# Kernel optimization log

Measured on AMD Instinct MI355X. Metric: run time of the kernel, lower is better.

Reference implementation:

```python
import math
import jax, jax.numpy as jnp
import numpy as np

# ---- static config ----
B, S, HID = 2, 8192, 1024
H, D = 8, 128                      # num_heads, head_dim = hidden // heads
CHUNK = 128                        # attention_chunk_size
PAST = 128 - 1                     # attention_context_left - 1
FUT = 128                          # attention_context_right
CTX = CHUNK + PAST + FUT           # 383
POS = CTX + 1                      # relative position table length (rel_shift pads to CTX+1)
CAP = 50.0                         # attention_logit_cap
Q_SCALE = D ** (-0.5) / math.log(2.0)
K_SCALE = math.log1p(math.e) / math.log(2.0)
NB = S // CHUNK                    # 64 blocks (S divisible by chunk -> no tail padding)


def setup_inputs() -> dict:
    key = jax.random.key(0)
    ks = jax.random.split(key, 8)
    s = 0.02
    return {
        "hidden_states": jax.random.normal(ks[0], (B, S, HID), jnp.float32),
        "position_embeddings": jax.random.normal(ks[1], (POS, HID), jnp.float32),
        "Wq": jax.random.normal(ks[2], (HID, H * D), jnp.float32) * s,
        "Wk": jax.random.normal(ks[3], (HID, H * D), jnp.float32) * s,
        "Wv": jax.random.normal(ks[4], (HID, H * D), jnp.float32) * s,
        "Wrel": jax.random.normal(ks[5], (HID, H * D), jnp.float32) * s,
        "Wpost": jax.random.normal(ks[6], (HID, HID), jnp.float32) * s,
        "per_dim_scale": jax.random.normal(ks[7], (D,), jnp.float32) * 0.1,
    }


def reference(hidden_states, position_embeddings, Wq, Wk, Wv, Wrel, Wpost, per_dim_scale):
    # projections (clipped-linear clamps are +/-inf -> no-ops); bias-free linears
    q = (hidden_states @ Wq).reshape(B, S, H, D)
    k = (hidden_states @ Wk).reshape(B, S, H, D)
    v = (hidden_states @ Wv).reshape(B, S, H, D)

    q = q * (Q_SCALE * jax.nn.softplus(per_dim_scale))  # per-dim scaling fused into q
    k = k * K_SCALE

    # _convert_to_block: [B, NB, CHUNK, H, D] (S % CHUNK == 0 -> no pad)
    qb = q.reshape(B, NB, CHUNK, H, D)

    # _extract_block_context: pad (PAST, FUT + CHUNK - 1) then unfold window=CTX step=CHUNK
    pad = ((0, 0), (PAST, FUT + CHUNK - 1), (0, 0), (0, 0))
    kp = jnp.pad(k, pad)
    vp = jnp.pad(v, pad)
    idx = jnp.arange(NB)[:, None] * CHUNK + jnp.arange(CTX)[None, :]  # [NB, CTX]
    kc = kp[:, idx]  # [B, NB, CTX, H, D]
    vc = vp[:, idx]  # [B, NB, CTX, H, D]

    # relative keys: [POS, H, D]
    rel_k = (position_embeddings @ Wrel).reshape(POS, H, D)

    # content scores: [B, H, NB, CHUNK, CTX]
    ac = jnp.einsum('bnchd,bnkhd->bhnck', qb, kc)
    # position scores before shift: [B, H, NB, CHUNK, POS]
    bd = jnp.einsum('bnchd,phd->bhncp', qb, rel_k)
    # Transformer-XL rel_shift (POS == CTX+1 so pad amount is zero)
    bd = bd.reshape(B, H, NB, CHUNK * POS)[..., : CHUNK * CTX]
    bd = bd.reshape(B, H, NB, CHUNK, CTX)

    # tanh soft-cap + softmax (no attention_mask)
    logits = jnp.tanh((ac + bd) / CAP) * CAP
    attn = jax.nn.softmax(logits, axis=-1)

    # weighted values -> [B, NB, CHUNK, H, D] -> [B, S, HID]
    out = jnp.einsum('bhnck,bnkhd->bnchd', attn, vc).reshape(B, S, H * D)
    return out @ Wpost
```

## Files before the change

### kernel.cpp

```cpp
#include <hip/hip_runtime.h>
#include <cmath>


using bf16x8 = __attribute__((ext_vector_type(8))) short;
using f32x4  = __attribute__((ext_vector_type(4))) float;
using s16x4  = __attribute__((ext_vector_type(4))) short;

__device__ __forceinline__ short f2bf(float f) {
  unsigned u = __float_as_uint(f);
  u = (u + 0x7FFF + ((u >> 16) & 1)) >> 16;
  return (short)u;
}
__device__ __forceinline__ float bf2f(unsigned short s) {
  return __uint_as_float(((unsigned)s) << 16);
}

__device__ __forceinline__ void gl16(void* lds, const void* gptr) {
  __builtin_amdgcn_global_load_lds(
      (const __attribute__((address_space(1))) unsigned int*)gptr,
      (__attribute__((address_space(3))) unsigned int*)lds, 16, 0, 0);
}

__global__ void cvt_bf16_k(const float* __restrict__ in, short* __restrict__ out, int n) {
  int i = (blockIdx.x * 256 + threadIdx.x) * 4;
  if (i + 3 < n) {
    float4 v = *(const float4*)&in[i];
    s16x4 o;
    o[0] = f2bf(v.x); o[1] = f2bf(v.y); o[2] = f2bf(v.z); o[3] = f2bf(v.w);
    *(s16x4*)&out[i] = o;
  }
}

__global__ void wtrans_k(const float* __restrict__ W, short* __restrict__ Wt) {
  __shared__ float T[64 * 65];
  const int tid = threadIdx.x;
  const int bx = blockIdx.x, by = blockIdx.y;
#pragma unroll
  for (int it = 0; it < 4; ++it) {
    int ci = it * 256 + tid;
    int k = ci >> 4, n4 = (ci & 15) * 4;
    float4 v = *(const float4*)&W[(size_t)(by * 64 + k) * 1024 + bx * 64 + n4];
    T[k * 65 + n4 + 0] = v.x;
    T[k * 65 + n4 + 1] = v.y;
    T[k * 65 + n4 + 2] = v.z;
    T[k * 65 + n4 + 3] = v.w;
  }
  __syncthreads();
#pragma unroll
  for (int it = 0; it < 2; ++it) {
    int co = it * 256 + tid;
    int nn = co >> 3, k8 = (co & 7) * 8;
    bf16x8 o;
#pragma unroll
    for (int jj = 0; jj < 8; ++jj) o[jj] = f2bf(T[(k8 + jj) * 65 + nn]);
    *(bf16x8*)&Wt[(size_t)(bx * 64 + nn) * 1024 + by * 64 + k8] = o;
  }
}

__global__ void qscale_k(const float* __restrict__ pds, float* __restrict__ qs, double qsb) {
  int d = threadIdx.x;
  double x = (double)pds[d];
  qs[d] = (float)(qsb * log1p(exp(x)));
}

__global__ void vpadzero_k(short* __restrict__ vpadT) {
  int row = blockIdx.x;
  int t = threadIdx.x;
  int key = (t < 127) ? t : (8192 + t);
  vpadT[(size_t)row * 8448 + key] = 0;
}


__device__ __forceinline__ void stage_half(short* ldsb, const short* gbase, int tid) {
#pragma unroll
  for (int it = 0; it < 2; ++it) {
    int idx = it * 512 + tid;
    int r = idx >> 3;
    int slot = idx & 7;
    int src = (slot ^ (r & 7)) << 3;
    gl16((char*)ldsb + idx * 16, gbase + (size_t)r * 1024 + src);
  }
}

__device__ __forceinline__ bf16x8 frag_ld(const short* hb, int row, int ks, int q4) {
  int slot = (ks * 4 + q4) ^ (row & 7);
  return *(const bf16x8*)((const char*)hb + row * 128 + slot * 16);
}

__global__ __launch_bounds__(512, 2)
void qkv256_k(const short* __restrict__ A, const short* __restrict__ Bt3,
              short* __restrict__ q_bf, short* __restrict__ kpad,
              short* __restrict__ vpadT,
              const float* __restrict__ qsc, float kscale) {
  __shared__ __align__(16) short lds[65536];

  const int tid = threadIdx.x;
  const int lane = tid & 63, wid = tid >> 6;
  const int q4 = lane >> 4, l16 = lane & 15;
  const int wr = wid >> 2, wc = wid & 3;

  const int id = blockIdx.x;
  const int xcd = id & 7, local = id >> 3;
  const int mm = xcd * 8 + local / 12, nn = local % 12;
  const int m0 = mm * 256, n0 = nn * 256;

  const short* Abase = A + (size_t)m0 * 1024;
  const short* Bbase = Bt3 + (size_t)n0 * 1024;

  const f32x4 z4 = {0.f, 0.f, 0.f, 0.f};
  f32x4 acc[8][4];
#pragma unroll
  for (int i = 0; i < 8; ++i)
#pragma unroll
    for (int j = 0; j < 4; ++j) acc[i][j] = z4;

  stage_half(lds + 0 * 32768 + 0 * 8192, Abase, tid);
  stage_half(lds + 0 * 32768 + 1 * 8192, Abase + 128 * 1024, tid);
  stage_half(lds + 0 * 32768 + 2 * 8192, Bbase, tid);
  stage_half(lds + 0 * 32768 + 3 * 8192, Bbase + 128 * 1024, tid);
  stage_half(lds + 1 * 32768 + 2 * 8192, Bbase + 64, tid);
  stage_half(lds + 1 * 32768 + 3 * 8192, Bbase + 128 * 1024 + 64, tid);
  asm volatile("s_waitcnt vmcnt(4)" ::: "memory");
  __builtin_amdgcn_s_barrier();

  for (int kt = 0; kt < 16; ++kt) {
    const int buf = kt & 1;
    const short* Acur = lds + buf * 32768 + wr * 8192;
    const short* Bcur = lds + buf * 32768 + (2 + (wc >> 1)) * 8192;
    const int brow0 = (wc & 1) * 64;

    bf16x8 bfr[4][2];

    {
#pragma unroll
      for (int j = 0; j < 4; ++j)
#pragma unroll
        for (int ks = 0; ks < 2; ++ks)
          bfr[j][ks] = frag_ld(Bcur, brow0 + j * 16 + l16, ks, q4);
      bf16x8 afr[2][2];
#pragma unroll
      for (int m2 = 0; m2 < 2; ++m2)
#pragma unroll
        for (int ks = 0; ks < 2; ++ks)
          afr[m2][ks] = frag_ld(Acur, m2 * 16 + l16, ks, q4);
      if (kt < 15)
        stage_half(lds + (buf ^ 1) * 32768 + 0 * 8192, Abase + (size_t)(kt + 1) * 64, tid);
      asm volatile("s_waitcnt lgkmcnt(8)" ::: "memory");
      __builtin_amdgcn_s_barrier();
      asm volatile("s_waitcnt lgkmcnt(0)" ::: "memory");
      __builtin_amdgcn_s_setprio(1);
#pragma unroll
      for (int ks = 0; ks < 2; ++ks)
#pragma unroll
        for (int m2 = 0; m2 < 2; ++m2)
#pragma unroll
          for (int j = 0; j < 4; ++j)
            acc[m2][j] = __builtin_amdgcn_mfma_f32_16x16x32_bf16(
                afr[m2][ks], bfr[j][ks], acc[m2][j], 0, 0, 0);
      __builtin_amdgcn_s_setprio(0);
      __builtin_amdgcn_s_barrier();
    }

#pragma unroll
    for (int p = 1; p < 4; ++p) {
      bf16x8 afr[2][2];
#pragma unroll
      for (int m2 = 0; m2 < 2; ++m2)
#pragma unroll
        for (int ks = 0; ks < 2; ++ks)
          afr[m2][ks] = frag_ld(Acur, (p * 2 + m2) * 16 + l16, ks, q4);
      if (p == 1) {
        if (kt < 15)
          stage_half(lds + (buf ^ 1) * 32768 + 1 * 8192,
                     Abase + 128 * 1024 + (size_t)(kt + 1) * 64, tid);
      } else if (p == 2) {
        if (kt < 14)
          stage_half(lds + buf * 32768 + 2 * 8192, Bbase + (size_t)(kt + 2) * 64, tid);
      } else {
        if (kt < 14)
          stage_half(lds + buf * 32768 + 3 * 8192,
                     Bbase + 128 * 1024 + (size_t)(kt + 2) * 64, tid);
      }
      __builtin_amdgcn_s_barrier();
      asm volatile("s_waitcnt lgkmcnt(0)" ::: "memory");
      __builtin_amdgcn_s_setprio(1);
#pragma unroll
      for (int ks = 0; ks < 2; ++ks)
#pragma unroll
        for (int m2 = 0; m2 < 2; ++m2)
#pragma unroll
          for (int j = 0; j < 4; ++j)
            acc[p * 2 + m2][j] = __builtin_amdgcn_mfma_f32_16x16x32_bf16(
                afr[m2][ks], bfr[j][ks], acc[p * 2 + m2][j], 0, 0, 0);
      __builtin_amdgcn_s_setprio(0);
      if (p == 3) {
        if (kt < 14) asm volatile("s_waitcnt vmcnt(4)" ::: "memory");
        else         asm volatile("s_waitcnt vmcnt(0)" ::: "memory");
      }
      __builtin_amdgcn_s_barrier();
    }
  }

  const int w = n0 >> 10;
  const int cw = n0 & 1023;
  const int b = m0 >> 13;
  const int s_base = (m0 & 8191) + wr * 128;

  if (w == 0) {
    float qsv[4];
#pragma unroll
    for (int j = 0; j < 4; ++j) qsv[j] = qsc[(cw + wc * 64 + j * 16 + l16) & 127];
#pragma unroll
    for (int m = 0; m < 8; ++m)
#pragma unroll
      for (int j = 0; j < 4; ++j)
#pragma unroll
        for (int rg = 0; rg < 4; ++rg) {
          int s = s_base + m * 16 + q4 * 4 + rg;
          int col = cw + wc * 64 + j * 16 + l16;
          int h = col >> 7, d = col & 127;
          int n = s >> 7, c = s & 127;
          q_bf[((size_t)(((b * 64 + n) * 8 + h) * 128 + c)) * 128 + d] =
              f2bf(acc[m][j][rg] * qsv[j]);
        }
  } else if (w == 1) {
#pragma unroll
    for (int m = 0; m < 8; ++m)
#pragma unroll
      for (int j = 0; j < 4; ++j)
#pragma unroll
        for (int rg = 0; rg < 4; ++rg) {
          int s = s_base + m * 16 + q4 * 4 + rg;
          int col = cw + wc * 64 + j * 16 + l16;
          int h = col >> 7, d = col & 127;
          kpad[((size_t)(b * 8 + h) * 8448 + 127 + s) * 128 + d] =
              f2bf(acc[m][j][rg] * kscale);
        }
  } else {
    short* T = lds;
#pragma unroll
    for (int hh = 0; hh < 2; ++hh) {
      __syncthreads();
      if ((wc >> 1) == hh) {
#pragma unroll
        for (int m = 0; m < 8; ++m)
#pragma unroll
          for (int j = 0; j < 4; ++j)
#pragma unroll
            for (int rg = 0; rg < 4; ++rg) {
              int sl = wr * 128 + m * 16 + q4 * 4 + rg;
              int dl = (wc & 1) * 64 + j * 16 + l16;
              T[dl * 264 + sl] = f2bf(acc[m][j][rg]);
            }
      }
      __syncthreads();
      const int h = (cw >> 7) + hh;
#pragma unroll
      for (int it = 0; it < 8; ++it) {
        int co = it * 512 + tid;
        int dd = co >> 5, s8 = (co & 31) * 8;
        *(bf16x8*)&vpadT[((size_t)(b * 8 + h) * 128 + dd) * 8448 + 127 + (m0 & 8191) + s8] =
            *(const bf16x8*)&T[dd * 264 + s8];
      }
    }
  }
}

__global__ __launch_bounds__(512, 2)
void post256_k(const short* __restrict__ A, const short* __restrict__ Bt,
               float* __restrict__ outf) {
  __shared__ __align__(16) short lds[65536];

  const int tid = threadIdx.x;
  const int lane = tid & 63, wid = tid >> 6;
  const int q4 = lane >> 4, l16 = lane & 15;
  const int wr = wid >> 2, wc = wid & 3;

  const int id = blockIdx.x;
  const int xcd = id & 7, local = id >> 3;
  const int mm = xcd * 8 + (local >> 2), nn = local & 3;
  const int m0 = mm * 256, n0 = nn * 256;

  const short* Abase = A + (size_t)m0 * 1024;
  const short* Bbase = Bt + (size_t)n0 * 1024;

  const f32x4 z4 = {0.f, 0.f, 0.f, 0.f};
  f32x4 acc[8][4];
#pragma unroll
  for (int i = 0; i < 8; ++i)
#pragma unroll
    for (int j = 0; j < 4; ++j) acc[i][j] = z4;

  stage_half(lds + 0 * 32768 + 0 * 8192, Abase, tid);
  stage_half(lds + 0 * 32768 + 1 * 8192, Abase + 128 * 1024, tid);
  stage_half(lds + 0 * 32768 + 2 * 8192, Bbase, tid);
  stage_half(lds + 0 * 32768 + 3 * 8192, Bbase + 128 * 1024, tid);
  stage_half(lds + 1 * 32768 + 2 * 8192, Bbase + 64, tid);
  stage_half(lds + 1 * 32768 + 3 * 8192, Bbase + 128 * 1024 + 64, tid);
  asm volatile("s_waitcnt vmcnt(4)" ::: "memory");
  __builtin_amdgcn_s_barrier();

  for (int kt = 0; kt < 16; ++kt) {
    const int buf = kt & 1;
    const short* Acur = lds + buf * 32768 + wr * 8192;
    const short* Bcur = lds + buf * 32768 + (2 + (wc >> 1)) * 8192;
    const int brow0 = (wc & 1) * 64;

    bf16x8 bfr[4][2];

    {
#pragma unroll
      for (int j = 0; j < 4; ++j)
#pragma unroll
        for (int ks = 0; ks < 2; ++ks)
          bfr[j][ks] = frag_ld(Bcur, brow0 + j * 16 + l16, ks, q4);
      bf16x8 afr[2][2];
#pragma unroll
      for (int m2 = 0; m2 < 2; ++m2)
#pragma unroll
        for (int ks = 0; ks < 2; ++ks)
          afr[m2][ks] = frag_ld(Acur, m2 * 16 + l16, ks, q4);
      if (kt < 15)
        stage_half(lds + (buf ^ 1) * 32768 + 0 * 8192, Abase + (size_t)(kt + 1) * 64, tid);
      asm volatile("s_waitcnt lgkmcnt(8)" ::: "memory");
      __builtin_amdgcn_s_barrier();
      asm volatile("s_waitcnt lgkmcnt(0)" ::: "memory");
      __builtin_amdgcn_s_setprio(1);
#pragma unroll
      for (int ks = 0; ks < 2; ++ks)
#pragma unroll
        for (int m2 = 0; m2 < 2; ++m2)
#pragma unroll
          for (int j = 0; j < 4; ++j)
            acc[m2][j] = __builtin_amdgcn_mfma_f32_16x16x32_bf16(
                afr[m2][ks], bfr[j][ks], acc[m2][j], 0, 0, 0);
      __builtin_amdgcn_s_setprio(0);
      __builtin_amdgcn_s_barrier();
    }

#pragma unroll
    for (int p = 1; p < 4; ++p) {
      bf16x8 afr[2][2];
#pragma unroll
      for (int m2 = 0; m2 < 2; ++m2)
#pragma unroll
        for (int ks = 0; ks < 2; ++ks)
          afr[m2][ks] = frag_ld(Acur, (p * 2 + m2) * 16 + l16, ks, q4);
      if (p == 1) {
        if (kt < 15)
          stage_half(lds + (buf ^ 1) * 32768 + 1 * 8192,
                     Abase + 128 * 1024 + (size_t)(kt + 1) * 64, tid);
      } else if (p == 2) {
        if (kt < 14)
          stage_half(lds + buf * 32768 + 2 * 8192, Bbase + (size_t)(kt + 2) * 64, tid);
      } else {
        if (kt < 14)
          stage_half(lds + buf * 32768 + 3 * 8192,
                     Bbase + 128 * 1024 + (size_t)(kt + 2) * 64, tid);
      }
      __builtin_amdgcn_s_barrier();
      asm volatile("s_waitcnt lgkmcnt(0)" ::: "memory");
      __builtin_amdgcn_s_setprio(1);
#pragma unroll
      for (int ks = 0; ks < 2; ++ks)
#pragma unroll
        for (int m2 = 0; m2 < 2; ++m2)
#pragma unroll
          for (int j = 0; j < 4; ++j)
            acc[p * 2 + m2][j] = __builtin_amdgcn_mfma_f32_16x16x32_bf16(
                afr[m2][ks], bfr[j][ks], acc[p * 2 + m2][j], 0, 0, 0);
      __builtin_amdgcn_s_setprio(0);
      if (p == 3) {
        if (kt < 14) asm volatile("s_waitcnt vmcnt(4)" ::: "memory");
        else         asm volatile("s_waitcnt vmcnt(0)" ::: "memory");
      }
      __builtin_amdgcn_s_barrier();
    }
  }

#pragma unroll
  for (int m = 0; m < 8; ++m)
#pragma unroll
    for (int j = 0; j < 4; ++j)
#pragma unroll
      for (int rg = 0; rg < 4; ++rg) {
        const int row = m0 + wr * 128 + m * 16 + q4 * 4 + rg;
        const int col = n0 + wc * 64 + j * 16 + l16;
        outf[(size_t)row * 1024 + col] = acc[m][j][rg];
      }
}

__global__ __launch_bounds__(256, 2)
void rel_gemm_k(const short* __restrict__ A, const short* __restrict__ Bt,
                short* __restrict__ relk) {
  __shared__ __align__(16) short As[128 * 32];
  __shared__ __align__(16) short Bs[128 * 32];

  const int tid = threadIdx.x;
  const int lane = tid & 63, wid = tid >> 6;
  const int q4 = lane >> 4, l16 = lane & 15;
  const int wr = wid >> 1, wc = wid & 1;
  const int m0 = blockIdx.x * 128, n0 = blockIdx.y * 128;

  const f32x4 z4 = {0.f, 0.f, 0.f, 0.f};
  f32x4 acc[4][4];
#pragma unroll
  for (int i = 0; i < 4; ++i)
#pragma unroll
    for (int j = 0; j < 4; ++j) acc[i][j] = z4;

  const int r0 = tid >> 2, s0_ = (tid & 3) * 8;
  for (int kk = 0; kk < 1024; kk += 32) {
    __syncthreads();
    gl16(&As[tid * 8],         A  + (size_t)(m0 + r0) * 1024 + kk + s0_);
    gl16(&Bs[tid * 8],         Bt + (size_t)(n0 + r0) * 1024 + kk + s0_);
    gl16(&As[(256 + tid) * 8], A  + (size_t)(m0 + 64 + r0) * 1024 + kk + s0_);
    gl16(&Bs[(256 + tid) * 8], Bt + (size_t)(n0 + 64 + r0) * 1024 + kk + s0_);
    __syncthreads();
    bf16x8 af[4], bfv[4];
#pragma unroll
    for (int i = 0; i < 4; ++i)
      af[i] = *(const bf16x8*)&As[(wr * 64 + i * 16 + l16) * 32 + q4 * 8];
#pragma unroll
    for (int j = 0; j < 4; ++j)
      bfv[j] = *(const bf16x8*)&Bs[(wc * 64 + j * 16 + l16) * 32 + q4 * 8];
#pragma unroll
    for (int i = 0; i < 4; ++i)
#pragma unroll
      for (int j = 0; j < 4; ++j)
        acc[i][j] = __builtin_amdgcn_mfma_f32_16x16x32_bf16(af[i], bfv[j], acc[i][j], 0, 0, 0);
  }

#pragma unroll
  for (int i = 0; i < 4; ++i)
#pragma unroll
    for (int j = 0; j < 4; ++j)
#pragma unroll
      for (int rg = 0; rg < 4; ++rg) {
        const int row = m0 + wr * 64 + i * 16 + q4 * 4 + rg;
        const int col = n0 + wc * 64 + j * 16 + l16;
        int h = col >> 7, d = col & 127;
        relk[(size_t)(h * 384 + row) * 128 + d] = f2bf(acc[i][j][rg]);
      }
}

__global__ __launch_bounds__(256, 2)
void bd_gemm_k(const short* __restrict__ qb_b, const short* __restrict__ relk,
               short* __restrict__ bds) {
  __shared__ __align__(16) short As[128 * 32];
  __shared__ __align__(16) short Bs[128 * 32];
  const int tid = threadIdx.x;
  const int lane = tid & 63, wid = tid >> 6;
  const int q4 = lane >> 4, l16 = lane & 15;
  const int wr = wid >> 1, wc = wid & 1;
  const int p0 = blockIdx.x * 128;
  const int nh = blockIdx.y;
  const int h = nh & 7;
  const short* A = qb_b + (size_t)nh * 16384;
  const short* Bt = relk + (size_t)h * (384 * 128);
  short* bdo = bds + (size_t)nh * 49152;

  const f32x4 z4 = {0.f, 0.f, 0.f, 0.f};
  f32x4 acc[4][4];
#pragma unroll
  for (int i = 0; i < 4; ++i)
#pragma unroll
    for (int j = 0; j < 4; ++j) acc[i][j] = z4;

  const int r0 = tid >> 2, s0_ = (tid & 3) * 8;
  for (int kk = 0; kk < 128; kk += 32) {
    __syncthreads();
    gl16(&As[tid * 8],         A  + (size_t)r0 * 128 + kk + s0_);
    gl16(&Bs[tid * 8],         Bt + (size_t)(p0 + r0) * 128 + kk + s0_);
    gl16(&As[(256 + tid) * 8], A  + (size_t)(64 + r0) * 128 + kk + s0_);
    gl16(&Bs[(256 + tid) * 8], Bt + (size_t)(p0 + 64 + r0) * 128 + kk + s0_);
    __syncthreads();
    bf16x8 af[4], bfv[4];
#pragma unroll
    for (int i = 0; i < 4; ++i)
      af[i] = *(const bf16x8*)&As[(wr * 64 + i * 16 + l16) * 32 + q4 * 8];
#pragma unroll
    for (int j = 0; j < 4; ++j)
      bfv[j] = *(const bf16x8*)&Bs[(wc * 64 + j * 16 + l16) * 32 + q4 * 8];
#pragma unroll
    for (int i = 0; i < 4; ++i)
#pragma unroll
      for (int j = 0; j < 4; ++j)
        acc[i][j] = __builtin_amdgcn_mfma_f32_16x16x32_bf16(af[i], bfv[j], acc[i][j], 0, 0, 0);
  }

#pragma unroll
  for (int i = 0; i < 4; ++i)
#pragma unroll
    for (int j = 0; j < 4; ++j)
#pragma unroll
      for (int rg = 0; rg < 4; ++rg) {
        int r = wr * 64 + i * 16 + q4 * 4 + rg;
        int p = p0 + wc * 64 + j * 16 + l16;
        int t = r + p;
        int c = (t < 383) ? r : (r + 1);
        int k = (t < 383) ? t : (t - 383);
        if (c < 128) {
          int tt = k >> 7, jj = (k >> 4) & 7, ll = k & 15;
          int wa = c >> 5, ia = (c >> 4) & 1, qa = (c >> 2) & 3, ra = c & 3;
          bdo[((((size_t)tt * 8 + jj) * 256) + wa * 64 + qa * 16 + ll) * 8 + ia * 4 + ra] =
              f2bf(acc[i][j][rg]);
        }
      }
}

__global__ __launch_bounds__(256, 3)
void attn_k(const short* __restrict__ qb_b, const short* __restrict__ kpad,
            const short* __restrict__ vpadT, const short* __restrict__ bds,
            short* __restrict__ attnout, int b) {
  __shared__ __align__(16) short Ks[4 * 128 * 32];
  __shared__ __align__(16) short Ps[64 * 136];

  const int tid = threadIdx.x;
  const int lane = tid & 63, wid = tid >> 6;
  const int q4 = lane >> 4, l16 = lane & 15;
  const int bx = blockIdx.x;
  const int qh = bx & 1, nh = bx >> 1;
  const int n = nh >> 3, h = nh & 7;

  const short* qtile = qb_b + (size_t)nh * 16384 + qh * 64 * 128;
  const short* kbase = kpad + ((size_t)(b * 8 + h) * 8448 + n * 128) * 128;
  const short* vtb = vpadT + (size_t)(b * 8 + h) * 128 * 8448 + n * 128;
  const short* bdb = bds + (size_t)nh * 49152;

#pragma unroll
  for (int it = 0; it < 4; ++it) {
    int ci = it * 256 + tid;
    int dc = ci >> 8, rr = (ci >> 2) & 63, sub = (ci & 3) * 8;
    gl16(&Ks[ci * 8], qtile + rr * 128 + dc * 32 + sub);
  }
  __syncthreads();
  bf16x8 qf[4];
#pragma unroll
  for (int dc = 0; dc < 4; ++dc)
    qf[dc] = *(const bf16x8*)&Ks[dc * 2048 + (wid * 16 + l16) * 32 + q4 * 8];

  const f32x4 z4 = {0.f, 0.f, 0.f, 0.f};
  f32x4 acco[8];
#pragma unroll
  for (int j = 0; j < 8; ++j) acco[j] = z4;
  float rsum[4] = {};

  for (int t = 0; t < 3; ++t) {
    __syncthreads();
#pragma unroll
    for (int it = 0; it < 8; ++it) {
      int ci = it * 256 + tid;
      int dc = ci >> 9, rr = (ci >> 2) & 127, sub = (ci & 3) * 8;
      gl16(&Ks[ci * 8], kbase + (size_t)(t * 128 + rr) * 128 + dc * 32 + sub);
    }

    s16x4 bdv[8];
#pragma unroll
    for (int j = 0; j < 8; ++j)
      bdv[j] = *(const s16x4*)&bdb[((((size_t)t * 8 + j) * 256) +
                 (qh * 2 + (wid >> 1)) * 64 + q4 * 16 + l16) * 8 + (wid & 1) * 4];

    __syncthreads();

    f32x4 accs[8];
#pragma unroll
    for (int j = 0; j < 8; ++j) accs[j] = z4;
#pragma unroll
    for (int dc = 0; dc < 4; ++dc) {
      bf16x8 kf[8];
#pragma unroll
      for (int j = 0; j < 8; ++j)
        kf[j] = *(const bf16x8*)&Ks[dc * 4096 + (j * 16 + l16) * 32 + q4 * 8];
#pragma unroll
      for (int j = 0; j < 8; ++j)
        accs[j] = __builtin_amdgcn_mfma_f32_16x16x32_bf16(qf[dc], kf[j], accs[j], 0, 0, 0);
    }

#pragma unroll
    for (int j = 0; j < 8; ++j) {
      const int kg = t * 128 + j * 16 + l16;
#pragma unroll
      for (int rg = 0; rg < 4; ++rg) {
        float sv = accs[j][rg] + bf2f((unsigned short)bdv[j][rg]);
        float tt = exp2f(sv * 0.057707801635558534f);
        float wgt = exp2f(-144.26950408889634f * __fdividef(1.0f, tt + 1.0f));
        wgt = (kg < 383) ? wgt : 0.0f;
        accs[j][rg] = wgt;
        rsum[rg] += wgt;
      }
    }
    __syncthreads();

#pragma unroll
    for (int it = 0; it < 8; ++it) {
      int ci = it * 256 + tid;
      int kc = ci >> 9, dd = (ci >> 2) & 127, sub = (ci & 3) * 8;
      gl16(&Ks[ci * 8], vtb + (size_t)dd * 8448 + t * 128 + kc * 32 + sub);
    }
#pragma unroll
    for (int j = 0; j < 8; ++j)
#pragma unroll
      for (int rg = 0; rg < 4; ++rg) {
        int c = wid * 16 + q4 * 4 + rg;
        int kl = j * 16 + l16;
        Ps[c * 136 + kl] = f2bf(accs[j][rg]);
      }
    __syncthreads();

#pragma unroll
    for (int kc = 0; kc < 4; ++kc) {
      bf16x8 pf, vf[8];
      pf = *(const bf16x8*)&Ps[(wid * 16 + l16) * 136 + kc * 32 + q4 * 8];
#pragma unroll
      for (int j = 0; j < 8; ++j)
        vf[j] = *(const bf16x8*)&Ks[kc * 4096 + (j * 16 + l16) * 32 + q4 * 8];
#pragma unroll
      for (int j = 0; j < 8; ++j)
        acco[j] = __builtin_amdgcn_mfma_f32_16x16x32_bf16(pf, vf[j], acco[j], 0, 0, 0);
    }
  }

  float rinv[4];
#pragma unroll
  for (int rg = 0; rg < 4; ++rg) {
    float rs = rsum[rg];
    rs += __shfl_xor(rs, 1);
    rs += __shfl_xor(rs, 2);
    rs += __shfl_xor(rs, 4);
    rs += __shfl_xor(rs, 8);
    rinv[rg] = __fdividef(1.0f, rs);
  }
#pragma unroll
  for (int j = 0; j < 8; ++j)
#pragma unroll
    for (int rg = 0; rg < 4; ++rg) {
      int srow = n * 128 + qh * 64 + wid * 16 + q4 * 4 + rg;
      int col = h * 128 + j * 16 + l16;
      attnout[((size_t)b * 8192 + srow) * 1024 + col] = f2bf(acco[j][rg] * rinv[rg]);
    }
}

extern "C" void kernel_launch(void* const* d_in, const int* in_sizes, int n_in,
                              void* d_out, int out_size, void* d_ws, size_t ws_size,
                              hipStream_t stream) {
  (void)in_sizes; (void)n_in; (void)out_size; (void)ws_size;
  const float* hs    = (const float*)d_in[0];
  const float* pemb  = (const float*)d_in[1];
  const float* Wq    = (const float*)d_in[2];
  const float* Wk    = (const float*)d_in[3];
  const float* Wv    = (const float*)d_in[4];
  const float* Wrel  = (const float*)d_in[5];
  const float* Wpost = (const float*)d_in[6];
  const float* pds   = (const float*)d_in[7];
  float* out = (float*)d_out;

  char* w = (char*)d_ws;
  auto alloc = [&](size_t bytes) -> char* {
    char* p = w; w += (bytes + 255) & ~(size_t)255; return p;
  };
  short* hs_bf   = (short*)alloc((size_t)16384 * 1024 * 2);
  short* pos_bf  = (short*)alloc((size_t)384 * 1024 * 2);
  short* Wq_t    = (short*)alloc((size_t)1024 * 1024 * 2);
  short* Wk_t    = (short*)alloc((size_t)1024 * 1024 * 2);
  short* Wv_t    = (short*)alloc((size_t)1024 * 1024 * 2);
  short* Wrel_t  = (short*)alloc((size_t)1024 * 1024 * 2);
  short* Wpost_t = (short*)alloc((size_t)1024 * 1024 * 2);
  float* qsc     = (float*)alloc(512);
  short* q_bf    = (short*)alloc((size_t)2 * 64 * 8 * 128 * 128 * 2);
  short* kpad    = (short*)alloc((size_t)2 * 8 * 8448 * 128 * 2);
  short* vpadT   = (short*)alloc((size_t)2 * 8 * 128 * 8448 * 2);
  short* relk    = (short*)alloc((size_t)8 * 384 * 128 * 2);
  short* bds     = (short*)alloc((size_t)64 * 8 * 128 * 384 * 2);
  short* attnout = hs_bf;

  const float kscale = (float)(log1p(exp(1.0)) / log(2.0));
  const double qsb = (1.0 / sqrt(128.0)) / log(2.0);

  cvt_bf16_k<<<16384, 256, 0, stream>>>(hs, hs_bf, 16384 * 1024);
  cvt_bf16_k<<<384, 256, 0, stream>>>(pemb, pos_bf, 384 * 1024);
  dim3 tg(16, 16);
  wtrans_k<<<tg, 256, 0, stream>>>(Wq, Wq_t);
  wtrans_k<<<tg, 256, 0, stream>>>(Wk, Wk_t);
  wtrans_k<<<tg, 256, 0, stream>>>(Wv, Wv_t);
  wtrans_k<<<tg, 256, 0, stream>>>(Wrel, Wrel_t);
  wtrans_k<<<tg, 256, 0, stream>>>(Wpost, Wpost_t);
  qscale_k<<<1, 128, 0, stream>>>(pds, qsc, qsb);
  hipMemsetAsync(kpad, 0, (size_t)2 * 8 * 8448 * 128 * 2, stream);
  vpadzero_k<<<2048, 256, 0, stream>>>(vpadT);

  qkv256_k<<<768, 512, 0, stream>>>(hs_bf, Wq_t, q_bf, kpad, vpadT, qsc, kscale);
  rel_gemm_k<<<dim3(3, 8), 256, 0, stream>>>(pos_bf, Wrel_t, relk);

  for (int b = 0; b < 2; ++b) {
    const short* qb_b = q_bf + (size_t)b * 64 * 8 * 128 * 128;
    bd_gemm_k<<<dim3(3, 512), 256, 0, stream>>>(qb_b, relk, bds);
    attn_k<<<1024, 256, 0, stream>>>(qb_b, kpad, vpadT, bds, attnout, b);
  }

  post256_k<<<256, 512, 0, stream>>>(attnout, Wpost_t, out);
}
```

Baseline: 505.2 us.

## Double-buffer K and V tiles in attention kernel with prefetch and manual waitcnts

Gives V its own LDS buffer so the V load for a tile is issued before the QK^T MFMAs and the next K tile is prefetched during softmax and PV. Replaces __syncthreads with explicit s_waitcnt vmcnt/lgkmcnt and s_barrier, and raises wave priority around the MFMA loops. The P buffer uses an XOR swizzle instead of padding. LDS use roughly doubles, so launch bounds drop from 3 to 2 blocks per CU, trading occupancy for overlap. Correctness now depends on the hand-written vmcnt counts.

```diff
diff --git a/kernel.cpp b/kernel.cpp
--- a/kernel.cpp
+++ b/kernel.cpp
@@ -509,12 +509,13 @@
       }
 }
 
-__global__ __launch_bounds__(256, 3)
+__global__ __launch_bounds__(256, 2)
 void attn_k(const short* __restrict__ qb_b, const short* __restrict__ kpad,
             const short* __restrict__ vpadT, const short* __restrict__ bds,
             short* __restrict__ attnout, int b) {
   __shared__ __align__(16) short Ks[4 * 128 * 32];
-  __shared__ __align__(16) short Ps[64 * 136];
+  __shared__ __align__(16) short Vs[4 * 128 * 32];
+  __shared__ __align__(16) short Ps[64 * 128];
 
   const int tid = threadIdx.x;
   const int lane = tid & 63, wid = tid >> 6;
@@ -532,13 +533,21 @@
   for (int it = 0; it < 4; ++it) {
     int ci = it * 256 + tid;
     int dc = ci >> 8, rr = (ci >> 2) & 63, sub = (ci & 3) * 8;
-    gl16(&Ks[ci * 8], qtile + rr * 128 + dc * 32 + sub);
-  }
-  __syncthreads();
+    gl16(&Ps[ci * 8], qtile + rr * 128 + dc * 32 + sub);
+  }
+#pragma unroll
+  for (int it = 0; it < 8; ++it) {
+    int ci = it * 256 + tid;
+    int dc = ci >> 9, rr = (ci >> 2) & 127, sub = (ci & 3) * 8;
+    gl16(&Ks[ci * 8], kbase + (size_t)rr * 128 + dc * 32 + sub);
+  }
+  asm volatile("s_waitcnt vmcnt(8)" ::: "memory");
+  asm volatile("s_barrier" ::: "memory");
   bf16x8 qf[4];
 #pragma unroll
   for (int dc = 0; dc < 4; ++dc)
-    qf[dc] = *(const bf16x8*)&Ks[dc * 2048 + (wid * 16 + l16) * 32 + q4 * 8];
+    qf[dc] = *(const bf16x8*)&Ps[dc * 2048 + (wid * 16 + l16) * 32 + q4 * 8];
+  asm volatile("s_waitcnt lgkmcnt(0)" ::: "memory");
 
   const f32x4 z4 = {0.f, 0.f, 0.f, 0.f};
   f32x4 acco[8];
@@ -546,26 +555,31 @@
   for (int j = 0; j < 8; ++j) acco[j] = z4;
   float rsum[4] = {};
 
+#pragma unroll
   for (int t = 0; t < 3; ++t) {
-    __syncthreads();
-#pragma unroll
-    for (int it = 0; it < 8; ++it) {
-      int ci = it * 256 + tid;
-      int dc = ci >> 9, rr = (ci >> 2) & 127, sub = (ci & 3) * 8;
-      gl16(&Ks[ci * 8], kbase + (size_t)(t * 128 + rr) * 128 + dc * 32 + sub);
-    }
+    asm volatile("s_barrier" ::: "memory");
 
     s16x4 bdv[8];
 #pragma unroll
     for (int j = 0; j < 8; ++j)
       bdv[j] = *(const s16x4*)&bdb[((((size_t)t * 8 + j) * 256) +
                  (qh * 2 + (wid >> 1)) * 64 + q4 * 16 + l16) * 8 + (wid & 1) * 4];
-
-    __syncthreads();
+    asm volatile("" ::: "memory");
+
+#pragma unroll
+    for (int it = 0; it < 8; ++it) {
+      int ci = it * 256 + tid;
+      int kc = ci >> 9, dd = (ci >> 2) & 127, sub = (ci & 3) * 8;
+      gl16(&Vs[ci * 8], vtb + (size_t)dd * 8448 + t * 128 + kc * 32 + sub);
+    }
+
+    asm volatile("s_waitcnt vmcnt(8)" ::: "memory");
+    asm volatile("s_barrier" ::: "memory");
 
     f32x4 accs[8];
 #pragma unroll
     for (int j = 0; j < 8; ++j) accs[j] = z4;
+    __builtin_amdgcn_s_setprio(1);
 #pragma unroll
     for (int dc = 0; dc < 4; ++dc) {
       bf16x8 kf[8];
@@ -576,6 +590,7 @@
       for (int j = 0; j < 8; ++j)
         accs[j] = __builtin_amdgcn_mfma_f32_16x16x32_bf16(qf[dc], kf[j], accs[j], 0, 0, 0);
     }
+    __builtin_amdgcn_s_setprio(0);
 
 #pragma unroll
     for (int j = 0; j < 8; ++j) {
@@ -590,35 +605,48 @@
         rsum[rg] += wgt;
       }
     }
-    __syncthreads();
-
-#pragma unroll
-    for (int it = 0; it < 8; ++it) {
-      int ci = it * 256 + tid;
-      int kc = ci >> 9, dd = (ci >> 2) & 127, sub = (ci & 3) * 8;
-      gl16(&Ks[ci * 8], vtb + (size_t)dd * 8448 + t * 128 + kc * 32 + sub);
-    }
+
+    asm volatile("s_barrier" ::: "memory");
+
+    if (t < 2) {
+#pragma unroll
+      for (int it = 0; it < 8; ++it) {
+        int ci = it * 256 + tid;
+        int dc = ci >> 9, rr = (ci >> 2) & 127, sub = (ci & 3) * 8;
+        gl16(&Ks[ci * 8], kbase + (size_t)((t + 1) * 128 + rr) * 128 + dc * 32 + sub);
+      }
+    }
+
 #pragma unroll
     for (int j = 0; j < 8; ++j)
 #pragma unroll
       for (int rg = 0; rg < 4; ++rg) {
         int c = wid * 16 + q4 * 4 + rg;
         int kl = j * 16 + l16;
-        Ps[c * 136 + kl] = f2bf(accs[j][rg]);
-      }
-    __syncthreads();
-
+        int g = (kl >> 3) ^ (c & 7);
+        Ps[c * 128 + g * 8 + (kl & 7)] = f2bf(accs[j][rg]);
+      }
+
+    if (t < 2) asm volatile("s_waitcnt vmcnt(8)" ::: "memory");
+    else       asm volatile("s_waitcnt vmcnt(0)" ::: "memory");
+    asm volatile("s_waitcnt lgkmcnt(0)" ::: "memory");
+    asm volatile("s_barrier" ::: "memory");
+
+    __builtin_amdgcn_s_setprio(1);
 #pragma unroll
     for (int kc = 0; kc < 4; ++kc) {
-      bf16x8 pf, vf[8];
-      pf = *(const bf16x8*)&Ps[(wid * 16 + l16) * 136 + kc * 32 + q4 * 8];
+      int c = wid * 16 + l16;
+      int g = (kc * 4 + q4) ^ (c & 7);
+      bf16x8 pf = *(const bf16x8*)&Ps[c * 128 + g * 8];
+      bf16x8 vf[8];
 #pragma unroll
       for (int j = 0; j < 8; ++j)
-        vf[j] = *(const bf16x8*)&Ks[kc * 4096 + (j * 16 + l16) * 32 + q4 * 8];
+        vf[j] = *(const bf16x8*)&Vs[kc * 4096 + (j * 16 + l16) * 32 + q4 * 8];
 #pragma unroll
       for (int j = 0; j < 8; ++j)
         acco[j] = __builtin_amdgcn_mfma_f32_16x16x32_bf16(pf, vf[j], acco[j], 0, 0, 0);
     }
+    __builtin_amdgcn_s_setprio(0);
   }
 
   float rinv[4];
```

New measurement: 512.7 us. No clear change (+1.5%).
